# Kernel optimization log

Measured on AMD Instinct MI355X. Metric: run time of the kernel, lower is better.

The kernel has to match this reference:

```python
import jax, jax.numpy as jnp
import numpy as np

B, S, D, H = 2, 2048, 512, 8
HD = D // H
SPARSITY = 0.15
KTOP = max(1, int(S * SPARSITY))          # 307 important rows
HALF_WIN = min(32, S // 4) // 2           # 16 -> window |i-j| <= 16
RC = min(16, S // 8)                      # 16 random links per query token


def setup_inputs() -> dict:
    key = jax.random.key(0)
    ks = jax.random.split(key, 8)
    s = 0.02
    return {
        "x":  jax.random.normal(ks[0], (B, S, D), jnp.float32),
        "Wq": jax.random.normal(ks[1], (D, D), jnp.float32) * s,
        "bq": jnp.zeros((D,), jnp.float32),
        "Wk": jax.random.normal(ks[2], (D, D), jnp.float32) * s,
        "bk": jnp.zeros((D,), jnp.float32),
        "Wv": jax.random.normal(ks[3], (D, D), jnp.float32) * s,
        "bv": jnp.zeros((D,), jnp.float32),
        "Wo": jax.random.normal(ks[4], (D, D), jnp.float32) * s,
        "bo": jnp.zeros((D,), jnp.float32),
        "Ws1": jax.random.normal(ks[5], (D, D // 2), jnp.float32) * s,
        "bs1": jnp.zeros((D // 2,), jnp.float32),
        "Ws2": jax.random.normal(ks[6], (D // 2, 1), jnp.float32) * s,
        "bs2": jnp.zeros((1,), jnp.float32),
        # models torch.randperm(S)[:RC] per (b, i); duplicates are harmless for set-to-1
        "rand_idx": jax.random.randint(ks[7], (B, S, RC), 0, S, jnp.int32),
    }


def _sparse_mask(x, Ws1, bs1, Ws2, bs2, rand_idx):
    # importance scorer: Linear -> ReLU -> Linear -> Sigmoid, squeeze(-1)
    imp = jax.nn.sigmoid(jax.nn.relu(x @ Ws1 + bs1) @ Ws2 + bs2)[..., 0]  # [B,S]
    _, top_idx = jax.lax.top_k(imp, KTOP)                                  # [B,KTOP]
    brange = jnp.arange(B)
    row_imp = jnp.zeros((B, S), bool).at[brange[:, None], top_idx].set(True)
    idx = jnp.arange(S)
    win = jnp.abs(idx[:, None] - idx[None, :]) <= HALF_WIN                 # [S,S]
    rmask = jnp.zeros((B, S, S), bool).at[
        brange[:, None, None], idx[None, :, None], rand_idx].set(True)    # [B,S,S]
    mask = row_imp[:, :, None] | win[None, :, :] | rmask                   # [B,S,S]
    tril = idx[:, None] >= idx[None, :]                                    # causal (mask * (causal==0))
    return mask & tril


def reference(x, Wq, bq, Wk, bk, Wv, bv, Wo, bo, Ws1, bs1, Ws2, bs2, rand_idx):
    allowed = _sparse_mask(x, Ws1, bs1, Ws2, bs2, rand_idx)                # [B,S,S] bool
    q = (x @ Wq + bq).reshape(B, S, H, HD).transpose(0, 2, 1, 3)           # [B,H,S,HD]
    k = (x @ Wk + bk).reshape(B, S, H, HD).transpose(0, 2, 1, 3)
    v = (x @ Wv + bv).reshape(B, S, H, HD).transpose(0, 2, 1, 3)
    scores = jnp.einsum('bhid,bhjd->bhij', q, k) / jnp.sqrt(jnp.float32(HD))
    scores = jnp.where(allowed[:, None, :, :], scores, -jnp.inf)
    attn = jax.nn.softmax(scores, axis=-1)                                 # every row has j=i allowed
    out = jnp.einsum('bhij,bhjd->bhid', attn, v)
    out = out.transpose(0, 2, 1, 3).reshape(B, S, D)
    return out @ Wo + bo
```

## Files before the change

kernel.cpp:

```cpp
#include <hip/hip_runtime.h>
#include <math.h>

typedef unsigned short u16;
typedef unsigned int u32;
typedef unsigned long long u64;
typedef short bf16x8 __attribute__((ext_vector_type(8)));
typedef float f32x4 __attribute__((ext_vector_type(4)));

constexpr int NB = 2, NS = 2048, ND = 512, NH = 8, NHD = 64;
constexpr int NKTOP = 307, NHWIN = 16, NRC = 16;
constexpr int NILIST = 320;
constexpr int NSPAR = NS - NKTOP;
constexpr int NSPAD = 1744;
constexpr int NCHUNK = 16;
constexpr int LDSK64 = 72;
constexpr int PSTR = 72;
constexpr int NSPB = (NSPAD / 4) * NH * NB;
constexpr int NMRG = NKTOP * NH * NB / 4;

__device__ __forceinline__ u16 f2bf(float f) {
  u32 u = __builtin_bit_cast(u32, f);
  u32 r = (u + 0x7FFFu + ((u >> 16) & 1u)) >> 16;
  return (u16)r;
}
__device__ __forceinline__ float bf2f(short v) {
  return __builtin_bit_cast(float, (u32)(u16)v << 16);
}

__global__ __launch_bounds__(256) void csa_prep(const float* __restrict__ W0, const float* __restrict__ W1,
                                                const float* __restrict__ W2, const float* __restrict__ W3,
                                                u16* __restrict__ wt, const float* __restrict__ x,
                                                u16* __restrict__ xb, const float* __restrict__ Ws1,
                                                const float* __restrict__ bs1, const float* __restrict__ Ws2,
                                                float* __restrict__ part) {
  __shared__ float sh[2 * 64 * 68];
  const int tid = threadIdx.x;
  if (blockIdx.x < 256) {
    const int m0 = (blockIdx.x & 63) * 64, n0 = (blockIdx.x >> 6) * 64;
    float(*As)[68] = (float(*)[68])sh;
    float(*Bs)[68] = (float(*)[68])(sh + 64 * 68);
    const int ty = tid >> 4, tx = tid & 15;
    float acc[4][4] = {};
    const int arow = tid & 63, aks = (tid >> 6) * 16;
    const int bk = tid >> 2, bc = (tid & 3) * 16;
    for (int k0 = 0; k0 < ND; k0 += 64) {
      __syncthreads();
      for (int g = 0; g < 4; g++) {
        float4 a = *(const float4*)(&x[(size_t)(m0 + arow) * ND + k0 + aks + g * 4]);
        As[aks + g * 4 + 0][arow] = a.x;
        As[aks + g * 4 + 1][arow] = a.y;
        As[aks + g * 4 + 2][arow] = a.z;
        As[aks + g * 4 + 3][arow] = a.w;
      }
      for (int g = 0; g < 4; g++)
        *(float4*)(&Bs[bk][bc + g * 4]) = *(const float4*)(&Ws1[(size_t)(k0 + bk) * 256 + n0 + bc + g * 4]);
      __syncthreads();
      for (int k = 0; k < 64; k++) {
        float4 av = *(const float4*)(&As[k][ty * 4]);
        float4 bv = *(const float4*)(&Bs[k][tx * 4]);
        float aa[4] = {av.x, av.y, av.z, av.w};
        float bb[4] = {bv.x, bv.y, bv.z, bv.w};
        for (int i = 0; i < 4; i++)
          for (int j = 0; j < 4; j++)
            acc[i][j] += aa[i] * bb[j];
      }
    }
    float4 w2 = *(const float4*)(&Ws2[n0 + tx * 4]);
    float4 b1 = *(const float4*)(&bs1[n0 + tx * 4]);
    for (int i = 0; i < 4; i++) {
      float p = fmaxf(acc[i][0] + b1.x, 0.f) * w2.x + fmaxf(acc[i][1] + b1.y, 0.f) * w2.y +
                fmaxf(acc[i][2] + b1.z, 0.f) * w2.z + fmaxf(acc[i][3] + b1.w, 0.f) * w2.w;
      for (int off = 1; off < 16; off <<= 1) p += __shfl_xor(p, off, 64);
      if (tx == 0) part[(size_t)(m0 + ty * 4 + i) * 4 + (blockIdx.x >> 6)] = p;
    }
  } else if (blockIdx.x < 768) {
    const int cb = blockIdx.x - 256;
    const int w = cb >> 7;
    const int kb = ((cb & 127) >> 4) * 64;
    const int nb = (cb & 15) * 32;
    const float* src = (w == 0) ? W0 : (w == 1) ? W1 : (w == 2) ? W2 : W3;
    float(*tile)[33] = (float(*)[33])sh;
    int tx = tid & 31, ty = tid >> 5;
    for (int i = ty; i < 64; i += 8) tile[i][tx] = src[(size_t)(kb + i) * ND + nb + tx];
    __syncthreads();
    u16* dst = wt + (size_t)w * ND * ND;
    for (int n = ty; n < 32; n += 8) {
      u32 pk = (u32)f2bf(tile[2 * tx][n]) | ((u32)f2bf(tile[2 * tx + 1][n]) << 16);
      *(u32*)(&dst[(size_t)(nb + n) * ND + kb + 2 * tx]) = pk;
    }
  } else {
    const int i = ((blockIdx.x - 768) * 256 + tid) * 8;
    float4 v0 = *(const float4*)(x + i);
    float4 v1 = *(const float4*)(x + i + 4);
    u32 o0 = (u32)f2bf(v0.x) | ((u32)f2bf(v0.y) << 16);
    u32 o1 = (u32)f2bf(v0.z) | ((u32)f2bf(v0.w) << 16);
    u32 o2 = (u32)f2bf(v1.x) | ((u32)f2bf(v1.y) << 16);
    u32 o3 = (u32)f2bf(v1.z) | ((u32)f2bf(v1.w) << 16);
    uint4 o = {o0, o1, o2, o3};
    *(uint4*)(xb + i) = o;
  }
}

__global__ __launch_bounds__(256) void csa_rank(const float* __restrict__ part, int* __restrict__ rowimp) {
  __shared__ float vals[NS];
  const int b = blockIdx.y;
  {
    int t8 = threadIdx.x * 8;
    for (int e = 0; e < 8; e++) {
      float4 pp = *(const float4*)(&part[(size_t)(b * NS + t8 + e) * 4]);
      vals[t8 + e] = (pp.x + pp.y) + (pp.z + pp.w);
    }
  }
  __syncthreads();
  const int wave = threadIdx.x >> 6, lane = threadIdx.x & 63;
  const int s0 = blockIdx.x * 8 + wave * 2;
  const int s1 = s0 + 1;
  const float v0 = vals[s0], v1 = vals[s1];
  int r0 = 0, r1 = 0;
  for (int t = lane; t < NS; t += 64) {
    float u = vals[t];
    r0 += (int)((u > v0) | ((u == v0) & (t < s0)));
    r1 += (int)((u > v1) | ((u == v1) & (t < s1)));
  }
  for (int off = 1; off < 64; off <<= 1) {
    r0 += __shfl_xor(r0, off, 64);
    r1 += __shfl_xor(r1, off, 64);
  }
  if (lane == 0) {
    rowimp[b * NS + s0] = (r0 < NKTOP) ? 1 : 0;
    rowimp[b * NS + s1] = (r1 < NKTOP) ? 1 : 0;
  }
}

__global__ __launch_bounds__(256) void csa_gemm_qkv(const u16* __restrict__ xb, const u16* __restrict__ Bt,
                                                    const float* __restrict__ bq, const float* __restrict__ bk,
                                                    const float* __restrict__ bv, u16* __restrict__ qb,
                                                    u16* __restrict__ kb, u16* __restrict__ vtb,
                                                    u16* __restrict__ vb, const int* __restrict__ rowimp,
                                                    int* __restrict__ ilist, int* __restrict__ nlist) {
  __shared__ __attribute__((aligned(16))) u16 As[128 * LDSK64];
  __shared__ __attribute__((aligned(16))) u16 Bs[64 * LDSK64];
  const int tid = threadIdx.x;
  if (blockIdx.x >= 768) {
    int* cs = (int*)As;
    const int b = blockIdx.x - 768;
    const int t = tid;
    int flags[8], sum = 0;
    for (int k = 0; k < 8; k++) {
      flags[k] = rowimp[b * NS + t * 8 + k];
      sum += flags[k];
    }
    cs[t] = sum;
    __syncthreads();
    for (int off = 1; off < 256; off <<= 1) {
      int v = (t >= off) ? cs[t - off] : 0;
      __syncthreads();
      cs[t] += v;
      __syncthreads();
    }
    int pos = cs[t] - sum;
    for (int k = 0; k < 8; k++) {
      int r = t * 8 + k;
      if (flags[k]) ilist[b * NILIST + pos++] = r;
      else nlist[b * NSPAD + (r - pos)] = r;
    }
    if (t < NILIST - NKTOP) ilist[b * NILIST + NKTOP + t] = -1;
    if (t < NSPAD - NSPAR) nlist[b * NSPAD + NSPAR + t] = -1;
    return;
  }
  const int wave = tid >> 6, lane = tid & 63;
  const int quad = lane >> 4, col = lane & 15;
  const int hsw = blockIdx.x & 7;
  const int rest = blockIdx.x >> 3;
  const int w = rest >> 5;
  const int m0 = (rest & 31) * 128;
  const int n0 = (w * 8 + hsw) * 64;
  const f32x4 zf = {0.f, 0.f, 0.f, 0.f};
  f32x4 acc[2][4] = {{zf, zf, zf, zf}, {zf, zf, zf, zf}};
  const int sar = tid >> 1, sak = (tid & 1) * 32;
  const int sbr = tid >> 2, sbk = (tid & 3) * 16;
  for (int k0 = 0; k0 < ND; k0 += 64) {
    __syncthreads();
    {
      const u16* xp = &xb[(size_t)(m0 + sar) * ND + k0 + sak];
      u16* ap = &As[sar * LDSK64 + sak];
      *(uint4*)(ap) = *(const uint4*)(xp);
      *(uint4*)(ap + 8) = *(const uint4*)(xp + 8);
      *(uint4*)(ap + 16) = *(const uint4*)(xp + 16);
      *(uint4*)(ap + 24) = *(const uint4*)(xp + 24);
    }
    *(uint4*)(&Bs[sbr * LDSK64 + sbk]) = *(const uint4*)(&Bt[(size_t)(n0 + sbr) * ND + k0 + sbk]);
    *(uint4*)(&Bs[sbr * LDSK64 + sbk + 8]) = *(const uint4*)(&Bt[(size_t)(n0 + sbr) * ND + k0 + sbk + 8]);
    __syncthreads();
    bf16x8 af[2][2];
    for (int r = 0; r < 2; r++)
      for (int hh = 0; hh < 2; hh++)
        af[r][hh] = *(const bf16x8*)(&As[(wave * 32 + r * 16 + col) * LDSK64 + hh * 32 + quad * 8]);
    for (int c = 0; c < 4; c++) {
      bf16x8 b0 = *(const bf16x8*)(&Bs[(c * 16 + col) * LDSK64 + quad * 8]);
      bf16x8 b1 = *(const bf16x8*)(&Bs[(c * 16 + col) * LDSK64 + 32 + quad * 8]);
      acc[0][c] = __builtin_amdgcn_mfma_f32_16x16x32_bf16(af[0][0], b0, acc[0][c], 0, 0, 0);
      acc[0][c] = __builtin_amdgcn_mfma_f32_16x16x32_bf16(af[0][1], b1, acc[0][c], 0, 0, 0);
      acc[1][c] = __builtin_amdgcn_mfma_f32_16x16x32_bf16(af[1][0], b0, acc[1][c], 0, 0, 0);
      acc[1][c] = __builtin_amdgcn_mfma_f32_16x16x32_bf16(af[1][1], b1, acc[1][c], 0, 0, 0);
    }
  }
  const float* bias = (w == 0) ? bq : (w == 1) ? bk : bv;
  for (int c = 0; c < 4; c++) {
    const int ng = n0 + c * 16 + col;
    const int nn = ng & 511, hh = nn >> 6, hd = nn & 63;
    const float bvv = bias[nn];
    for (int r = 0; r < 2; r++) {
      for (int rr = 0; rr < 4; rr++) {
        const int m = m0 + wave * 32 + r * 16 + quad * 4 + rr;
        const int bb = m >> 11, s = m & (NS - 1);
        u16 v16 = f2bf(acc[r][c][rr] + bvv);
        if (w == 0) qb[((size_t)(bb * NH + hh) * NS + s) * NHD + hd] = v16;
        else if (w == 1) kb[((size_t)(bb * NH + hh) * NS + s) * NHD + hd] = v16;
        else {
          vtb[((size_t)(bb * NH + hh) * NHD + hd) * NS + s] = v16;
          vb[((size_t)(bb * NH + hh) * NS + s) * NHD + hd] = v16;
        }
      }
    }
  }
}

__global__ __launch_bounds__(256) void csa_gemm_out(const u16* __restrict__ A, const u16* __restrict__ Bt,
                                                    const float* __restrict__ bias, float* __restrict__ outp) {
  __shared__ __attribute__((aligned(16))) u16 As[64 * LDSK64];
  __shared__ __attribute__((aligned(16))) u16 Bs[64 * LDSK64];
  const int tid = threadIdx.x;
  const int wave = tid >> 6, lane = tid & 63;
  const int quad = lane >> 4, col = lane & 15;
  const int m0 = blockIdx.x * 64;
  const int n0 = blockIdx.y * 64;
  const f32x4 zf = {0.f, 0.f, 0.f, 0.f};
  f32x4 acc[4] = {zf, zf, zf, zf};
  const int sr = tid >> 2, sk = (tid & 3) * 16;
  for (int k0 = 0; k0 < ND; k0 += 64) {
    __syncthreads();
    *(uint4*)(&As[sr * LDSK64 + sk]) = *(const uint4*)(&A[(size_t)(m0 + sr) * ND + k0 + sk]);
    *(uint4*)(&As[sr * LDSK64 + sk + 8]) = *(const uint4*)(&A[(size_t)(m0 + sr) * ND + k0 + sk + 8]);
    *(uint4*)(&Bs[sr * LDSK64 + sk]) = *(const uint4*)(&Bt[(size_t)(n0 + sr) * ND + k0 + sk]);
    *(uint4*)(&Bs[sr * LDSK64 + sk + 8]) = *(const uint4*)(&Bt[(size_t)(n0 + sr) * ND + k0 + sk + 8]);
    __syncthreads();
    bf16x8 af0 = *(const bf16x8*)(&As[(wave * 16 + col) * LDSK64 + quad * 8]);
    bf16x8 af1 = *(const bf16x8*)(&As[(wave * 16 + col) * LDSK64 + 32 + quad * 8]);
    for (int nt = 0; nt < 4; nt++) {
      bf16x8 bf0 = *(const bf16x8*)(&Bs[(nt * 16 + col) * LDSK64 + quad * 8]);
      bf16x8 bf1 = *(const bf16x8*)(&Bs[(nt * 16 + col) * LDSK64 + 32 + quad * 8]);
      acc[nt] = __builtin_amdgcn_mfma_f32_16x16x32_bf16(af0, bf0, acc[nt], 0, 0, 0);
      acc[nt] = __builtin_amdgcn_mfma_f32_16x16x32_bf16(af1, bf1, acc[nt], 0, 0, 0);
    }
  }
  for (int nt = 0; nt < 4; nt++) {
    const int n = n0 + nt * 16 + col;
    const float bvv = bias[n];
    for (int r = 0; r < 4; r++) {
      const int m = m0 + wave * 16 + quad * 4 + r;
      outp[(size_t)m * ND + n] = acc[nt][r] + bvv;
    }
  }
}

__global__ __launch_bounds__(64) void csa_attn_imp(const u16* __restrict__ qb, const u16* __restrict__ kb,
                                                   const u16* __restrict__ vtb, const int* __restrict__ ilist,
                                                   float* __restrict__ pbuf) {
  const int lane = threadIdx.x;
  const int quad = lane >> 4, col = lane & 15;
  const int h = blockIdx.x & 7;
  const int b = (blockIdx.x >> 3) & 1;
  const int rest = blockIdx.x >> 4;
  const int qt = rest % (NILIST / 16);
  const int chunk = rest / (NILIST / 16);
  const int bh = b * NH + h;

  const int* il = ilist + b * NILIST;
  const u16* qptr = qb + (size_t)(b * NH + h) * NS * NHD;
  const u16* kptr = kb + (size_t)(b * NH + h) * NS * NHD;
  const u16* vptr = vtb + (size_t)(b * NH + h) * NHD * NS;

  const int iq = il[qt * 16 + col];
  const int qrow = (iq < 0) ? 0 : iq;
  bf16x8 qf0 = *(const bf16x8*)(qptr + qrow * NHD + quad * 8);
  bf16x8 qf1 = *(const bf16x8*)(qptr + qrow * NHD + 32 + quad * 8);

  const f32x4 zf = {0.f, 0.f, 0.f, 0.f};
  float m_r[4], l_r[4];
  f32x4 of[4];
  int irow[4];
  for (int r = 0; r < 4; r++) {
    m_r[r] = -INFINITY;
    l_r[r] = 0.f;
    irow[r] = il[qt * 16 + quad * 4 + r];
  }
  for (int n = 0; n < 4; n++) of[n] = zf;

  __shared__ __attribute__((aligned(16))) u16 Pl[16 * PSTR];

  const int max_i = il[(qt * 16 + 15 > NKTOP - 1) ? (NKTOP - 1) : (qt * 16 + 15)];
  const int ntiles = (max_i >> 6) + 1;
  for (int t = chunk; t < ntiles; t += NCHUNK) {
    const int j0 = t * 64;
    f32x4 cg[4];
    for (int g = 0; g < 4; g++) {
      const int jb = j0 + g * 16;
      bf16x8 k0f = *(const bf16x8*)(kptr + (jb + col) * NHD + quad * 8);
      bf16x8 k1f = *(const bf16x8*)(kptr + (jb + col) * NHD + 32 + quad * 8);
      f32x4 c = zf;
      c = __builtin_amdgcn_mfma_f32_16x16x32_bf16(qf0, k0f, c, 0, 0, 0);
      c = __builtin_amdgcn_mfma_f32_16x16x32_bf16(qf1, k1f, c, 0, 0, 0);
      cg[g] = c;
    }
    float ps[4][4], alpha[4];
    for (int r = 0; r < 4; r++) {
      const int i = irow[r];
      float s[4];
      float vmax = -INFINITY;
      for (int g = 0; g < 4; g++) {
        s[g] = (j0 + g * 16 + col <= i) ? cg[g][r] * 0.125f : -INFINITY;
        vmax = fmaxf(vmax, s[g]);
      }
      for (int off = 1; off < 16; off <<= 1) vmax = fmaxf(vmax, __shfl_xor(vmax, off, 64));
      float newm = fmaxf(m_r[r], vmax);
      bool dead = (newm == -INFINITY);
      float a = dead ? 1.f : __expf(m_r[r] - newm);
      float psum = 0.f;
      for (int g = 0; g < 4; g++) {
        float p = dead ? 0.f : __expf(s[g] - newm);
        ps[r][g] = p;
        psum += p;
      }
      for (int off = 1; off < 16; off <<= 1) psum += __shfl_xor(psum, off, 64);
      m_r[r] = newm;
      l_r[r] = l_r[r] * a + psum;
      alpha[r] = a;
    }
    for (int n = 0; n < 4; n++)
      for (int r = 0; r < 4; r++) of[n][r] *= alpha[r];
    __syncthreads();
    for (int r = 0; r < 4; r++)
      for (int g = 0; g < 4; g++)
        Pl[(quad * 4 + r) * PSTR + g * 16 + col] = f2bf(ps[r][g]);
    __syncthreads();
    bf16x8 pf0 = *(const bf16x8*)(&Pl[col * PSTR + quad * 8]);
    bf16x8 pf1 = *(const bf16x8*)(&Pl[col * PSTR + 32 + quad * 8]);
    for (int vn = 0; vn < 4; vn++) {
      bf16x8 vf0 = *(const bf16x8*)(vptr + (size_t)(vn * 16 + col) * NS + j0 + quad * 8);
      bf16x8 vf1 = *(const bf16x8*)(vptr + (size_t)(vn * 16 + col) * NS + j0 + 32 + quad * 8);
      of[vn] = __builtin_amdgcn_mfma_f32_16x16x32_bf16(pf0, vf0, of[vn], 0, 0, 0);
      of[vn] = __builtin_amdgcn_mfma_f32_16x16x32_bf16(pf1, vf1, of[vn], 0, 0, 0);
    }
  }
  float* pr = pbuf + ((size_t)(bh * NCHUNK + chunk) * NILIST + qt * 16) * 66;
  for (int r = 0; r < 4; r++) {
    const int row = quad * 4 + r;
    if (col == 0) {
      pr[row * 66 + 0] = m_r[r];
      pr[row * 66 + 1] = l_r[r];
    }
    for (int vn = 0; vn < 4; vn++)
      pr[row * 66 + 2 + vn * 16 + col] = of[vn][r];
  }
}

__global__ __launch_bounds__(256) void csa_attn_sparse(const u16* __restrict__ qb, const u16* __restrict__ kb,
                                                       const u16* __restrict__ vb, const int* __restrict__ nlist,
                                                       const int* __restrict__ rand_idx,
                                                       const float* __restrict__ pbuf,
                                                       const int* __restrict__ ilist, u16* __restrict__ attnb) {
  __shared__ __attribute__((aligned(16))) u16 ql[4][64];
  __shared__ float pl[4][33];
  __shared__ int jl[4][33];
  const int wave = threadIdx.x >> 6, lane = threadIdx.x & 63;
  if (blockIdx.x >= NSPB) {
    const int mu = (blockIdx.x - NSPB) * 4 + wave;
    const int kp = mu % NKTOP;
    const int h = (mu / NKTOP) & 7;
    const int b = mu / (NKTOP * NH);
    const int z = b * NH + h;
    float mstar = -INFINITY;
    for (int c = 0; c < NCHUNK; c++)
      mstar = fmaxf(mstar, pbuf[((size_t)(z * NCHUNK + c) * NILIST + kp) * 66]);
    float lsum = 0.f, osum = 0.f;
    for (int c = 0; c < NCHUNK; c++) {
      const float* base = pbuf + ((size_t)(z * NCHUNK + c) * NILIST + kp) * 66;
      float mc = base[0];
      float w = (mc == -INFINITY) ? 0.f : __expf(mc - mstar);
      lsum += w * base[1];
      osum += w * base[2 + lane];
    }
    const int i = ilist[b * NILIST + kp];
    attnb[((size_t)(b * NS + i) * NH + h) * NHD + lane] = f2bf(osum / lsum);
    return;
  }
  const int h = blockIdx.x & 7;
  const int b = (blockIdx.x >> 3) & 1;
  const int slot = (blockIdx.x >> 4) * 4 + wave;
  const int i = nlist[b * NSPAD + slot];
  const int iv = (i < 0) ? 0 : i;

  const u16* qrow = qb + ((size_t)(b * NH + h) * NS + iv) * NHD;
  const u16* kbase = kb + (size_t)(b * NH + h) * NS * NHD;
  const u16* vbase = vb + (size_t)(b * NH + h) * NS * NHD;

  if (lane < 8) *(bf16x8*)(&ql[wave][lane * 8]) = *(const bf16x8*)(qrow + lane * 8);
  __syncthreads();

  float sd = bf2f((short)ql[wave][lane]) * bf2f((short)kbase[(size_t)iv * NHD + lane]);
  for (int off = 1; off < 64; off <<= 1) sd += __shfl_xor(sd, off, 64);
  sd *= 0.125f;

  const int c = lane >> 1, half = lane & 1;
  int j, valid;
  if (c < 16) {
    j = i - NHWIN + c;
    valid = (j >= 0);
  } else {
    const int* rr = rand_idx + ((size_t)b * NS + iv) * NRC;
    const int cr = c - 16;
    j = rr[cr];
    valid = (j <= i - NHWIN - 1);
    for (int cp = 0; cp < cr; cp++) valid &= (rr[cp] != j);
  }
  const int jr = valid ? j : 0;
  float s = 0.f;
  {
    const u16* krow = kbase + (size_t)jr * NHD + half * 32;
    for (int c8 = 0; c8 < 4; c8++) {
      bf16x8 kv = *(const bf16x8*)(krow + c8 * 8);
      bf16x8 qv = *(const bf16x8*)(&ql[wave][half * 32 + c8 * 8]);
      for (int e = 0; e < 8; e++) s += bf2f(qv[e]) * bf2f(kv[e]);
    }
  }
  s += __shfl_xor(s, 1, 64);
  s = valid ? s * 0.125f : -INFINITY;

  float smax = s;
  for (int off = 1; off < 64; off <<= 1) smax = fmaxf(smax, __shfl_xor(smax, off, 64));
  smax = fmaxf(smax, sd);
  float p = valid ? __expf(s - smax) : 0.f;
  float pd = __expf(sd - smax);
  float pm = (half == 0) ? p : 0.f;
  for (int off = 1; off < 64; off <<= 1) pm += __shfl_xor(pm, off, 64);
  const float lsum = pm + pd;

  if (half == 0) {
    pl[wave][c] = p;
    jl[wave][c] = jr;
  }
  if (lane == 0) {
    pl[wave][32] = pd;
    jl[wave][32] = iv;
  }
  __syncthreads();

  float o = 0.f;
  for (int jj = 0; jj < 33; jj++) {
    const int jk = __builtin_amdgcn_readfirstlane(jl[wave][jj]);
    const float pj = pl[wave][jj];
    o += pj * bf2f((short)vbase[(size_t)jk * NHD + lane]);
  }
  if (i >= 0)
    attnb[((size_t)(b * NS + i) * NH + h) * NHD + lane] = f2bf(o / lsum);
}

extern "C" void kernel_launch(void* const* d_in, const int* in_sizes, int n_in,
                              void* d_out, int out_size, void* d_ws, size_t ws_size,
                              hipStream_t stream) {
  const float* x = (const float*)d_in[0];
  const float* bq = (const float*)d_in[2];
  const float* bk = (const float*)d_in[4];
  const float* bv = (const float*)d_in[6];
  const float* bo = (const float*)d_in[8];
  const float* Ws1 = (const float*)d_in[9];
  const float* bs1 = (const float*)d_in[10];
  const float* Ws2 = (const float*)d_in[11];
  const int* rand_idx = (const int*)d_in[13];
  float* out = (float*)d_out;

  char* p = (char*)d_ws;
  u16* wt = (u16*)p;         p += (size_t)4 * ND * ND * 2;
  u16* xb = (u16*)p;         p += (size_t)NB * NS * ND * 2;
  u16* qbuf = (u16*)p;       p += (size_t)NB * NH * NS * NHD * 2;
  u16* kbuf = (u16*)p;       p += (size_t)NB * NH * NS * NHD * 2;
  u16* vtbuf = (u16*)p;      p += (size_t)NB * NH * NHD * NS * 2;
  u16* vbuf = (u16*)p;       p += (size_t)NB * NH * NS * NHD * 2;
  u16* attnb = (u16*)p;      p += (size_t)NB * NS * ND * 2;
  float* part = (float*)p;   p += (size_t)NB * NS * 4 * 4;
  int* rowimp = (int*)p;     p += (size_t)NB * NS * 4;
  int* ilist = (int*)p;      p += (size_t)NB * NILIST * 4;
  int* nlist = (int*)p;      p += (size_t)NB * NSPAD * 4;
  float* pbuf = (float*)p;

  csa_prep<<<dim3(1792), 256, 0, stream>>>((const float*)d_in[1], (const float*)d_in[3],
                                           (const float*)d_in[5], (const float*)d_in[7], wt,
                                           x, xb, Ws1, bs1, Ws2, part);
  csa_rank<<<dim3(NS / 8, NB), 256, 0, stream>>>(part, rowimp);

  csa_gemm_qkv<<<dim3(770), 256, 0, stream>>>(xb, wt, bq, bk, bv, qbuf, kbuf, vtbuf, vbuf,
                                              rowimp, ilist, nlist);

  csa_attn_imp<<<dim3((NILIST / 16) * NCHUNK * 16), 64, 0, stream>>>(qbuf, kbuf, vtbuf, ilist, pbuf);

  csa_attn_sparse<<<dim3(NSPB + NMRG), 256, 0, stream>>>(qbuf, kbuf, vbuf, nlist, rand_idx,
                                                         pbuf, ilist, attnb);

  csa_gemm_out<<<dim3(64, 8), 256, 0, stream>>>(attnb, wt + 3 * (size_t)ND * ND, bo, out);
}
```

Baseline: 194.2 us.

## Prefetch V rows early in sparse attention, use wave fences, enlarge output GEMM tile

In the sparse attention kernel, the key indices are written to LDS first so that all 33 V-row loads can be issued into registers before the score computation, overlapping their latency with the QK dot products and softmax. Block-wide __syncthreads are replaced with a per-wave LDS waitcnt plus wave barrier, since each wave only reads its own LDS slice. The output projection GEMM tile grows from 64 to 128 rows per block, halving the grid and reusing each loaded B tile across twice as many rows. The cost is more registers for the prefetched V values and larger accumulators, which could lower occupancy.

```diff
diff --git a/kernel.cpp b/kernel.cpp
--- a/kernel.cpp
+++ b/kernel.cpp
@@ -25,6 +25,10 @@
 }
 __device__ __forceinline__ float bf2f(short v) {
   return __builtin_bit_cast(float, (u32)(u16)v << 16);
+}
+__device__ __forceinline__ void wave_lds_fence() {
+  __builtin_amdgcn_s_waitcnt(0xC07F);
+  __builtin_amdgcn_wave_barrier();
 }
 
 __global__ __launch_bounds__(256) void csa_prep(const float* __restrict__ W0, const float* __restrict__ W1,
@@ -228,38 +232,51 @@
 
 __global__ __launch_bounds__(256) void csa_gemm_out(const u16* __restrict__ A, const u16* __restrict__ Bt,
                                                     const float* __restrict__ bias, float* __restrict__ outp) {
-  __shared__ __attribute__((aligned(16))) u16 As[64 * LDSK64];
+  __shared__ __attribute__((aligned(16))) u16 As[128 * LDSK64];
   __shared__ __attribute__((aligned(16))) u16 Bs[64 * LDSK64];
   const int tid = threadIdx.x;
   const int wave = tid >> 6, lane = tid & 63;
   const int quad = lane >> 4, col = lane & 15;
-  const int m0 = blockIdx.x * 64;
+  const int m0 = blockIdx.x * 128;
   const int n0 = blockIdx.y * 64;
   const f32x4 zf = {0.f, 0.f, 0.f, 0.f};
-  f32x4 acc[4] = {zf, zf, zf, zf};
-  const int sr = tid >> 2, sk = (tid & 3) * 16;
+  f32x4 acc[2][4] = {{zf, zf, zf, zf}, {zf, zf, zf, zf}};
+  const int sar = tid >> 1, sak = (tid & 1) * 32;
+  const int sbr = tid >> 2, sbk = (tid & 3) * 16;
   for (int k0 = 0; k0 < ND; k0 += 64) {
     __syncthreads();
-    *(uint4*)(&As[sr * LDSK64 + sk]) = *(const uint4*)(&A[(size_t)(m0 + sr) * ND + k0 + sk]);
-    *(uint4*)(&As[sr * LDSK64 + sk + 8]) = *(const uint4*)(&A[(size_t)(m0 + sr) * ND + k0 + sk + 8]);
-    *(uint4*)(&Bs[sr * LDSK64 + sk]) = *(const uint4*)(&Bt[(size_t)(n0 + sr) * ND + k0 + sk]);
-    *(uint4*)(&Bs[sr * LDSK64 + sk + 8]) = *(const uint4*)(&Bt[(size_t)(n0 + sr) * ND + k0 + sk + 8]);
-    __syncthreads();
-    bf16x8 af0 = *(const bf16x8*)(&As[(wave * 16 + col) * LDSK64 + quad * 8]);
-    bf16x8 af1 = *(const bf16x8*)(&As[(wave * 16 + col) * LDSK64 + 32 + quad * 8]);
-    for (int nt = 0; nt < 4; nt++) {
-      bf16x8 bf0 = *(const bf16x8*)(&Bs[(nt * 16 + col) * LDSK64 + quad * 8]);
-      bf16x8 bf1 = *(const bf16x8*)(&Bs[(nt * 16 + col) * LDSK64 + 32 + quad * 8]);
-      acc[nt] = __builtin_amdgcn_mfma_f32_16x16x32_bf16(af0, bf0, acc[nt], 0, 0, 0);
-      acc[nt] = __builtin_amdgcn_mfma_f32_16x16x32_bf16(af1, bf1, acc[nt], 0, 0, 0);
-    }
-  }
-  for (int nt = 0; nt < 4; nt++) {
-    const int n = n0 + nt * 16 + col;
+    {
+      const u16* xp = &A[(size_t)(m0 + sar) * ND + k0 + sak];
+      u16* ap = &As[sar * LDSK64 + sak];
+      *(uint4*)(ap) = *(const uint4*)(xp);
+      *(uint4*)(ap + 8) = *(const uint4*)(xp + 8);
+      *(uint4*)(ap + 16) = *(const uint4*)(xp + 16);
+      *(uint4*)(ap + 24) = *(const uint4*)(xp + 24);
+    }
+    *(uint4*)(&Bs[sbr * LDSK64 + sbk]) = *(const uint4*)(&Bt[(size_t)(n0 + sbr) * ND + k0 + sbk]);
+    *(uint4*)(&Bs[sbr * LDSK64 + sbk + 8]) = *(const uint4*)(&Bt[(size_t)(n0 + sbr) * ND + k0 + sbk + 8]);
+    __syncthreads();
+    bf16x8 af[2][2];
+    for (int r = 0; r < 2; r++)
+      for (int hh = 0; hh < 2; hh++)
+        af[r][hh] = *(const bf16x8*)(&As[(wave * 32 + r * 16 + col) * LDSK64 + hh * 32 + quad * 8]);
+    for (int c = 0; c < 4; c++) {
+      bf16x8 b0 = *(const bf16x8*)(&Bs[(c * 16 + col) * LDSK64 + quad * 8]);
+      bf16x8 b1 = *(const bf16x8*)(&Bs[(c * 16 + col) * LDSK64 + 32 + quad * 8]);
+      acc[0][c] = __builtin_amdgcn_mfma_f32_16x16x32_bf16(af[0][0], b0, acc[0][c], 0, 0, 0);
+      acc[0][c] = __builtin_amdgcn_mfma_f32_16x16x32_bf16(af[0][1], b1, acc[0][c], 0, 0, 0);
+      acc[1][c] = __builtin_amdgcn_mfma_f32_16x16x32_bf16(af[1][0], b0, acc[1][c], 0, 0, 0);
+      acc[1][c] = __builtin_amdgcn_mfma_f32_16x16x32_bf16(af[1][1], b1, acc[1][c], 0, 0, 0);
+    }
+  }
+  for (int c = 0; c < 4; c++) {
+    const int n = n0 + c * 16 + col;
     const float bvv = bias[n];
-    for (int r = 0; r < 4; r++) {
-      const int m = m0 + wave * 16 + quad * 4 + r;
-      outp[(size_t)m * ND + n] = acc[nt][r] + bvv;
+    for (int r = 0; r < 2; r++) {
+      for (int rr = 0; rr < 4; rr++) {
+        const int m = m0 + wave * 32 + r * 16 + quad * 4 + rr;
+        outp[(size_t)m * ND + n] = acc[r][c][rr] + bvv;
+      }
     }
   }
 }
@@ -406,11 +423,6 @@
   const u16* vbase = vb + (size_t)(b * NH + h) * NS * NHD;
 
   if (lane < 8) *(bf16x8*)(&ql[wave][lane * 8]) = *(const bf16x8*)(qrow + lane * 8);
-  __syncthreads();
-
-  float sd = bf2f((short)ql[wave][lane]) * bf2f((short)kbase[(size_t)iv * NHD + lane]);
-  for (int off = 1; off < 64; off <<= 1) sd += __shfl_xor(sd, off, 64);
-  sd *= 0.125f;
 
   const int c = lane >> 1, half = lane & 1;
   int j, valid;
@@ -425,6 +437,21 @@
     for (int cp = 0; cp < cr; cp++) valid &= (rr[cp] != j);
   }
   const int jr = valid ? j : 0;
+  if (half == 0) jl[wave][c] = jr;
+  if (lane == 0) jl[wave][32] = iv;
+  wave_lds_fence();
+
+  u16 vreg[33];
+#pragma unroll
+  for (int jj = 0; jj < 33; jj++) {
+    const int jk = __builtin_amdgcn_readfirstlane(jl[wave][jj]);
+    vreg[jj] = vbase[(size_t)jk * NHD + lane];
+  }
+
+  float sd = bf2f((short)ql[wave][lane]) * bf2f((short)kbase[(size_t)iv * NHD + lane]);
+  for (int off = 1; off < 64; off <<= 1) sd += __shfl_xor(sd, off, 64);
+  sd *= 0.125f;
+
   float s = 0.f;
   {
     const u16* krow = kbase + (size_t)jr * NHD + half * 32;
@@ -446,22 +473,14 @@
   for (int off = 1; off < 64; off <<= 1) pm += __shfl_xor(pm, off, 64);
   const float lsum = pm + pd;
 
-  if (half == 0) {
-    pl[wave][c] = p;
-    jl[wave][c] = jr;
-  }
-  if (lane == 0) {
-    pl[wave][32] = pd;
-    jl[wave][32] = iv;
-  }
-  __syncthreads();
+  if (half == 0) pl[wave][c] = p;
+  if (lane == 0) pl[wave][32] = pd;
+  wave_lds_fence();
 
   float o = 0.f;
-  for (int jj = 0; jj < 33; jj++) {
-    const int jk = __builtin_amdgcn_readfirstlane(jl[wave][jj]);
-    const float pj = pl[wave][jj];
-    o += pj * bf2f((short)vbase[(size_t)jk * NHD + lane]);
-  }
+#pragma unroll
+  for (int jj = 0; jj < 33; jj++)
+    o += pl[wave][jj] * bf2f((short)vreg[jj]);
   if (i >= 0)
     attnb[((size_t)(b * NS + i) * NH + h) * NHD + lane] = f2bf(o / lsum);
 }
@@ -507,5 +526,5 @@
   csa_attn_sparse<<<dim3(NSPB + NMRG), 256, 0, stream>>>(qbuf, kbuf, vbuf, nlist, rand_idx,
                                                          pbuf, ilist, attnb);
 
-  csa_gemm_out<<<dim3(64, 8), 256, 0, stream>>>(attnb, wt + 3 * (size_t)ND * ND, bo, out);
-}
+  csa_gemm_out<<<dim3(32, 8), 256, 0, stream>>>(attnb, wt + 3 * (size_t)ND * ND, bo, out);
+}
```

New measurement: 196.7 us. No clear change (+1.3%).
